# Kernel optimization log

Measured on AMD Instinct MI355X. Metric: run time of the kernel, lower is better.

The kernel has to match this reference:

```python
import jax, jax.numpy as jnp
import numpy as np

MAX_WORDS = 2048  # max word tokens per sequence (static num_segments)


def setup_inputs() -> dict:
    key = jax.random.key(0)
    k1, k2, k3, k4 = jax.random.split(key, 4)
    B, S, H, D = 8, 4096, 768, 1024
    embeddings = jax.random.normal(k1, (B, S, H), dtype=jnp.float32)
    proj_w = jax.random.normal(k2, (H, D), dtype=jnp.float32) * 0.02
    proj_b = jax.random.normal(k3, (D,), dtype=jnp.float32) * 0.02
    masks = jnp.ones((B, S), dtype=jnp.int32)
    word_ids = jnp.sort(jax.random.randint(k4, (B, S), 0, MAX_WORDS), axis=-1)
    return {"embeddings": embeddings, "proj_w": proj_w, "proj_b": proj_b,
            "masks": masks, "word_ids": word_ids}


def reference(embeddings, proj_w, proj_b, masks, word_ids):
    B, S, H = embeddings.shape
    W = MAX_WORDS
    # Flatten batch+word into one segment id space: seg in [0, B*W)
    seg = (word_ids + jnp.arange(B, dtype=word_ids.dtype)[:, None] * W).reshape(-1)
    flat_emb = embeddings.reshape(B * S, H)
    # segment-sum of embeddings over subwords of each word  -> (B, W, H)
    sum_emb = jax.ops.segment_sum(flat_emb, seg, num_segments=B * W).reshape(B, W, H)
    ones = jnp.ones((B * S,), dtype=jnp.float32)
    counts = jax.ops.segment_sum(ones, seg, num_segments=B * W).reshape(B, W)
    mcounts = jax.ops.segment_sum(masks.reshape(-1).astype(jnp.float32), seg,
                                  num_segments=B * W).reshape(B, W)
    # word is valid iff it has >=1 subword and ALL its subwords have mask==1
    valid = (counts > 0) & (counts == mcounts)
    mean_emb = sum_emb / jnp.maximum(counts, 1.0)[..., None]
    token_embeddings = jnp.where(valid[..., None], mean_emb, 0.0)  # (B, W, H)
    token_masks = valid.astype(jnp.int32)                          # (B, W)
    # projection: hidden 768 -> config.hidden_size 1024
    out = jnp.einsum('bwh,hd->bwd', token_embeddings, proj_w) + proj_b
    return out, token_masks
```

## Files before the change

### kernel.cpp

```cpp
#include <hip/hip_runtime.h>
#include <hip/hip_bf16.h>
#include <stdint.h>

#define Bn 8
#define Sn 4096
#define Hn 768
#define Dn 1024
#define Wn 2048

typedef __attribute__((ext_vector_type(8))) short short8;
typedef __attribute__((ext_vector_type(4))) short short4v;
typedef __attribute__((ext_vector_type(4))) float floatx4;

__device__ __forceinline__ void load_lds16(const void* g, void* l) {
  __builtin_amdgcn_global_load_lds(
      (const __attribute__((address_space(1))) void*)g,
      (__attribute__((address_space(3))) void*)l, 16, 0, 0);
}

__global__ __launch_bounds__(256) void k_transpose(const float* __restrict__ pw,
                                                   __hip_bfloat16* __restrict__ wb) {
  __shared__ float tile[32][33];
  const int d0 = blockIdx.x * 32, h0 = blockIdx.y * 32;
  const int tx = threadIdx.x, ty = threadIdx.y;
#pragma unroll
  for (int i = 0; i < 32; i += 8)
    tile[ty + i][tx] = pw[(size_t)(h0 + ty + i) * Dn + d0 + tx];
  __syncthreads();
#pragma unroll
  for (int i = 0; i < 32; i += 8)
    wb[(size_t)(d0 + ty + i) * Hn + h0 + tx] = (__hip_bfloat16)tile[tx][ty + i];
}

__global__ __launch_bounds__(256) void k_bounds(const int* __restrict__ wid,
                                                int* __restrict__ starts) {
  const int b = blockIdx.y;
  const int s = blockIdx.x * 256 + threadIdx.x;
  const int* wb = wid + (size_t)b * Sn;
  int* sb = starts + b * (Wn + 1);
  const int cur = wb[s];
  const int prev = (s == 0) ? -1 : wb[s - 1];
  for (int ww = prev + 1; ww <= cur; ++ww) sb[ww] = s;
  if (s == Sn - 1)
    for (int ww = cur + 1; ww <= Wn; ++ww) sb[ww] = Sn;
}

__global__ __launch_bounds__(256) void k_words(const float* __restrict__ emb,
                                               const int* __restrict__ masks,
                                               const int* __restrict__ starts,
                                               __hip_bfloat16* __restrict__ wa,
                                               float* __restrict__ out_masks) {
  const int b = blockIdx.y;
  const int wave = threadIdx.x >> 6, lane = threadIdx.x & 63;
  const int w = blockIdx.x * 4 + wave;

  const int* sb = starts + b * (Wn + 1);
  const int start = sb[w];
  const int end = sb[w + 1];
  const int count = end - start;

  int mcount = 0;
  const int* mb = masks + (size_t)b * Sn;
  for (int s = start; s < end; ++s) mcount += mb[s];
  const bool valid = (count > 0) && (count == mcount);
  const float inv = valid ? 1.0f / (float)count : 0.0f;

  floatx4 sum[3] = {{0.f, 0.f, 0.f, 0.f}, {0.f, 0.f, 0.f, 0.f}, {0.f, 0.f, 0.f, 0.f}};
  const float* eb = emb + (size_t)b * Sn * Hn;
  for (int s = start; s < end; ++s) {
    const floatx4* row = (const floatx4*)(eb + (size_t)s * Hn);
#pragma unroll
    for (int j = 0; j < 3; ++j) sum[j] += row[j * 64 + lane];
  }

  const size_t rowbase = ((size_t)b * Wn + w) * Hn;
#pragma unroll
  for (int j = 0; j < 3; ++j) {
    short4v o;
#pragma unroll
    for (int c = 0; c < 4; ++c) {
      __hip_bfloat16 h = (__hip_bfloat16)(sum[j][c] * inv);
      o[c] = *reinterpret_cast<short*>(&h);
    }
    *(short4v*)&wa[rowbase + (size_t)(j * 64 + lane) * 4] = o;
  }
  if (lane == 0) out_masks[(size_t)b * Wn + w] = valid ? 1.0f : 0.0f;
}

__global__ __launch_bounds__(256) void k_gemm(const short* __restrict__ A,
                                              const short* __restrict__ Bt,
                                              const float* __restrict__ bias,
                                              float* __restrict__ out) {
  constexpr int K = Hn;
  constexpr int N = Dn;
  __shared__ __align__(16) short lsA[128 * 32];
  __shared__ __align__(16) short lsB[128 * 32];

  const int t = threadIdx.x;
  const int lane = t & 63, wave = t >> 6;
  const int wm = wave >> 1, wn = wave & 1;
  const int lane16 = lane & 15, quad = lane >> 4;
  const int m0 = blockIdx.y * 128, n0 = blockIdx.x * 128;

  const int lrow = t >> 2;
  const int lcol = (t & 3) * 8;
  const short* gA0 = A + (size_t)(m0 + lrow) * K + lcol;
  const short* gB0 = Bt + (size_t)(n0 + lrow) * K + lcol;
  short* lA0 = &lsA[lrow * 32 + lcol];
  short* lB0 = &lsB[lrow * 32 + lcol];

  floatx4 acc[4][4];
#pragma unroll
  for (int i = 0; i < 4; ++i)
#pragma unroll
    for (int j = 0; j < 4; ++j) acc[i][j] = (floatx4){0.f, 0.f, 0.f, 0.f};

  for (int k0 = 0; k0 < K; k0 += 32) {
    load_lds16(gA0 + k0, lA0);
    load_lds16(gA0 + (size_t)64 * K + k0, lA0 + 64 * 32);
    load_lds16(gB0 + k0, lB0);
    load_lds16(gB0 + (size_t)64 * K + k0, lB0 + 64 * 32);
    __syncthreads();

    short8 af[4], bf[4];
#pragma unroll
    for (int mi = 0; mi < 4; ++mi)
      af[mi] = *(const short8*)&lsA[(wm * 64 + mi * 16 + lane16) * 32 + quad * 8];
#pragma unroll
    for (int ni = 0; ni < 4; ++ni)
      bf[ni] = *(const short8*)&lsB[(wn * 64 + ni * 16 + lane16) * 32 + quad * 8];

#pragma unroll
    for (int mi = 0; mi < 4; ++mi)
#pragma unroll
      for (int ni = 0; ni < 4; ++ni)
        acc[mi][ni] = __builtin_amdgcn_mfma_f32_16x16x32_bf16(af[mi], bf[ni], acc[mi][ni], 0, 0, 0);
    __syncthreads();
  }

#pragma unroll
  for (int mi = 0; mi < 4; ++mi) {
#pragma unroll
    for (int ni = 0; ni < 4; ++ni) {
      const int n = n0 + wn * 64 + ni * 16 + lane16;
      const float bv = bias[n];
#pragma unroll
      for (int r = 0; r < 4; ++r) {
        const int m = m0 + wm * 64 + mi * 16 + quad * 4 + r;
        out[(size_t)m * N + n] = acc[mi][ni][r] + bv;
      }
    }
  }
}

extern "C" void kernel_launch(void* const* d_in, const int* in_sizes, int n_in,
                              void* d_out, int out_size, void* d_ws, size_t ws_size,
                              hipStream_t stream) {
  const float* emb    = (const float*)d_in[0];
  const float* proj_w = (const float*)d_in[1];
  const float* proj_b = (const float*)d_in[2];
  const int*   masks  = (const int*)d_in[3];
  const int*   wid    = (const int*)d_in[4];

  float* out = (float*)d_out;
  float* out_masks = out + (size_t)Bn * Wn * Dn;

  __hip_bfloat16* wb = (__hip_bfloat16*)d_ws;
  __hip_bfloat16* wa = wb + (size_t)Dn * Hn;
  int* starts = (int*)(wa + (size_t)Bn * Wn * Hn);

  dim3 g1(Dn / 32, Hn / 32), b1(32, 8);
  k_transpose<<<g1, b1, 0, stream>>>(proj_w, wb);

  dim3 gb(Sn / 256, Bn);
  k_bounds<<<gb, 256, 0, stream>>>(wid, starts);

  dim3 g2(Wn / 4, Bn);
  k_words<<<g2, 256, 0, stream>>>(emb, masks, starts, wa, out_masks);

  dim3 g3(Dn / 128, (Bn * Wn) / 128);
  k_gemm<<<g3, 256, 0, stream>>>((const short*)wa, (const short*)wb, proj_b, out);
}
```

Before: 224.2 us.

## Merge prep kernels, vectorize mask check, unroll segment sum, XCD-aware GEMM tiling

Combines the weight transpose and word-boundary kernels into one launch to save a kernel launch. In the word kernel, the serial per-word mask count becomes a lane-parallel all-ones check with a wave vote, and the subword accumulation is unrolled by two so more loads are in flight. The GEMM grid is flattened and remapped so that blocks landing on the same XCD share A-row tiles, which should improve L2 reuse. The mask check now tests mask==1 rather than comparing a sum to the count, which is equivalent only for 0/1 masks.

```diff
diff --git a/kernel.cpp b/kernel.cpp
--- a/kernel.cpp
+++ b/kernel.cpp
@@ -18,31 +18,34 @@
       (__attribute__((address_space(3))) void*)l, 16, 0, 0);
 }
 
-__global__ __launch_bounds__(256) void k_transpose(const float* __restrict__ pw,
-                                                   __hip_bfloat16* __restrict__ wb) {
-  __shared__ float tile[32][33];
-  const int d0 = blockIdx.x * 32, h0 = blockIdx.y * 32;
-  const int tx = threadIdx.x, ty = threadIdx.y;
+__global__ __launch_bounds__(256) void k_prep(const float* __restrict__ pw,
+                                              const int* __restrict__ wid,
+                                              __hip_bfloat16* __restrict__ wb,
+                                              int* __restrict__ starts) {
+  if (blockIdx.x < 768) {
+    __shared__ float tile[32][33];
+    const int bt = blockIdx.x;
+    const int d0 = (bt % 32) * 32, h0 = (bt / 32) * 32;
+    const int tx = threadIdx.x & 31, ty = threadIdx.x >> 5;
 #pragma unroll
-  for (int i = 0; i < 32; i += 8)
-    tile[ty + i][tx] = pw[(size_t)(h0 + ty + i) * Dn + d0 + tx];
-  __syncthreads();
+    for (int i = 0; i < 32; i += 8)
+      tile[ty + i][tx] = pw[(size_t)(h0 + ty + i) * Dn + d0 + tx];
+    __syncthreads();
 #pragma unroll
-  for (int i = 0; i < 32; i += 8)
-    wb[(size_t)(d0 + ty + i) * Hn + h0 + tx] = (__hip_bfloat16)tile[tx][ty + i];
-}
-
-__global__ __launch_bounds__(256) void k_bounds(const int* __restrict__ wid,
-                                                int* __restrict__ starts) {
-  const int b = blockIdx.y;
-  const int s = blockIdx.x * 256 + threadIdx.x;
-  const int* wb = wid + (size_t)b * Sn;
-  int* sb = starts + b * (Wn + 1);
-  const int cur = wb[s];
-  const int prev = (s == 0) ? -1 : wb[s - 1];
-  for (int ww = prev + 1; ww <= cur; ++ww) sb[ww] = s;
-  if (s == Sn - 1)
-    for (int ww = cur + 1; ww <= Wn; ++ww) sb[ww] = Sn;
+    for (int i = 0; i < 32; i += 8)
+      wb[(size_t)(d0 + ty + i) * Hn + h0 + tx] = (__hip_bfloat16)tile[tx][ty + i];
+  } else {
+    const int bid = blockIdx.x - 768;
+    const int g = bid * 256 + threadIdx.x;
+    const int b = g >> 12, s = g & (Sn - 1);
+    const int* wbi = wid + (size_t)b * Sn;
+    int* sb = starts + b * (Wn + 1);
+    const int cur = wbi[s];
+    const int prev = (s == 0) ? -1 : wbi[s - 1];
+    for (int ww = prev + 1; ww <= cur; ++ww) sb[ww] = s;
+    if (s == Sn - 1)
+      for (int ww = cur + 1; ww <= Wn; ++ww) sb[ww] = Sn;
+  }
 }
 
 __global__ __launch_bounds__(256) void k_words(const float* __restrict__ emb,
@@ -59,18 +62,30 @@
   const int end = sb[w + 1];
   const int count = end - start;
 
-  int mcount = 0;
   const int* mb = masks + (size_t)b * Sn;
-  for (int s = start; s < end; ++s) mcount += mb[s];
-  const bool valid = (count > 0) && (count == mcount);
+  bool allone = true;
+  for (int s0 = start; s0 < end; s0 += 64) {
+    const int idx = s0 + lane;
+    allone = allone && ((idx < end) ? (mb[idx] == 1) : true);
+  }
+  const bool valid = (count > 0) && __all(allone);
   const float inv = valid ? 1.0f / (float)count : 0.0f;
 
   floatx4 sum[3] = {{0.f, 0.f, 0.f, 0.f}, {0.f, 0.f, 0.f, 0.f}, {0.f, 0.f, 0.f, 0.f}};
   const float* eb = emb + (size_t)b * Sn * Hn;
-  for (int s = start; s < end; ++s) {
-    const floatx4* row = (const floatx4*)(eb + (size_t)s * Hn);
+  int s = start;
+  for (; s + 1 < end; s += 2) {
+    const floatx4* r0 = (const floatx4*)(eb + (size_t)s * Hn);
+    const floatx4* r1 = (const floatx4*)(eb + (size_t)(s + 1) * Hn);
 #pragma unroll
-    for (int j = 0; j < 3; ++j) sum[j] += row[j * 64 + lane];
+    for (int j = 0; j < 3; ++j) sum[j] += r0[j * 64 + lane];
+#pragma unroll
+    for (int j = 0; j < 3; ++j) sum[j] += r1[j * 64 + lane];
+  }
+  if (s < end) {
+    const floatx4* r0 = (const floatx4*)(eb + (size_t)s * Hn);
+#pragma unroll
+    for (int j = 0; j < 3; ++j) sum[j] += r0[j * 64 + lane];
   }
 
   const size_t rowbase = ((size_t)b * Wn + w) * Hn;
@@ -100,7 +115,12 @@
   const int lane = t & 63, wave = t >> 6;
   const int wm = wave >> 1, wn = wave & 1;
   const int lane16 = lane & 15, quad = lane >> 4;
-  const int m0 = blockIdx.y * 128, n0 = blockIdx.x * 128;
+
+  const int linear = blockIdx.x;
+  const int xcd = linear & 7;
+  const int o = linear >> 3;
+  const int m0 = (xcd * 16 + (o >> 3)) * 128;
+  const int n0 = (o & 7) * 128;
 
   const int lrow = t >> 2;
   const int lcol = (t & 3) * 8;
@@ -169,15 +189,9 @@
   __hip_bfloat16* wa = wb + (size_t)Dn * Hn;
   int* starts = (int*)(wa + (size_t)Bn * Wn * Hn);
 
-  dim3 g1(Dn / 32, Hn / 32), b1(32, 8);
-  k_transpose<<<g1, b1, 0, stream>>>(proj_w, wb);
+  k_prep<<<dim3(768 + (Bn * Sn) / 256), 256, 0, stream>>>(proj_w, wid, wb, starts);
 
-  dim3 gb(Sn / 256, Bn);
-  k_bounds<<<gb, 256, 0, stream>>>(wid, starts);
+  k_words<<<dim3(Wn / 4, Bn), 256, 0, stream>>>(emb, masks, starts, wa, out_masks);
 
-  dim3 g2(Wn / 4, Bn);
-  k_words<<<g2, 256, 0, stream>>>(emb, masks, starts, wa, out_masks);
-
-  dim3 g3(Dn / 128, (Bn * Wn) / 128);
-  k_gemm<<<g3, 256, 0, stream>>>((const short*)wa, (const short*)wb, proj_b, out);
+  k_gemm<<<dim3(1024), 256, 0, stream>>>((const short*)wa, (const short*)wb, proj_b, out);
 }
```

After: 210.9 us. 6.0% less time.
